# Kernel optimization log

Measured on AMD Instinct MI355X. Metric: run time of the kernel, lower is better.

Reference implementation:

```python
import jax, jax.numpy as jnp
import numpy as np

B, F, S, K = 4, 1024, 2048, 7


def _activate_norm(x):
    # relu -> mean-center over last dim -> L2-normalize scaled by sqrt(n)
    out = jax.nn.relu(x)
    out = out - jnp.mean(out, axis=-1, keepdims=True)
    n = out.shape[-1]
    denom = (jnp.sqrt(jnp.sum(out * out, axis=-1, keepdims=True)) + 1e-5) * (n ** -0.5)
    return out / denom


def _causal_conv(x, w, k):
    # x: [B, C_in, S], w: [C_out, C_in, k]; left-pad by k-1 for causality
    return jax.lax.conv_general_dilated(
        x, w, window_strides=(1,), padding=[(k - 1, 0)],
        dimension_numbers=('NCH', 'OIH', 'NCH'))


def _feed_forward(x, w0, w1, k):
    return _causal_conv(_activate_norm(_causal_conv(x, w0, k)), w1, k)


def setup_inputs() -> dict:
    key = jax.random.key(0)
    ks = jax.random.split(key, 8)
    scale = 0.02
    inp = jax.random.normal(ks[0], (B, F, S), dtype=jnp.float32)
    pos_embd = jax.random.normal(ks[1], (1, F, S), dtype=jnp.float32) * scale
    divisor = jnp.arange(1, F + 1, dtype=jnp.float32).reshape(1, F, 1)
    ws = [jax.random.normal(ks[2 + i], (F, F, K), dtype=jnp.float32) * scale
          for i in range(6)]
    return {
        'inp': inp, 'pos_embd': pos_embd, 'divisor': divisor,
        'depth_w0': ws[0], 'depth_w1': ws[1],
        'point_w0': ws[2], 'point_w1': ws[3],
        'shift_w0': ws[4], 'shift_w1': ws[5],
    }


def reference(inp, pos_embd, divisor, depth_w0, depth_w1, point_w0, point_w1, shift_w0, shift_w1):
    out = inp + pos_embd
    depth = _feed_forward(out, depth_w0, depth_w1, K)
    point = _feed_forward(out, point_w0, point_w1, K)
    shift = _feed_forward(out, shift_w0, shift_w1, K)
    # linear attention: cumsum over feature axis (dim 1), matching depth.cumsum(1)
    return _activate_norm(inp * (jnp.cumsum(depth, axis=1) / divisor + point) + shift)
```

## Files before the change

kernel.cpp:

```cpp
#include <hip/hip_runtime.h>
#include <hip/hip_bf16.h>
#include <stdint.h>

#define B_ 4
#define F_ 1024
#define S_ 2048
#define K_ 7
#define SP_ (S_ + K_ - 1)
#define FC_ 64
#define NC_ (F_ / FC_)
#define FF_ ((size_t)F_ * F_)
#define BFS_ ((size_t)B_ * F_ * S_)
#define BSPF_ ((size_t)B_ * SP_ * F_)
#define NT_ 112

using f32x4 = __attribute__((ext_vector_type(4))) float;
using s16x8 = __attribute__((ext_vector_type(8))) short;
using bf16 = __hip_bfloat16;

typedef const __attribute__((address_space(1))) void gvoid_t;
typedef __attribute__((address_space(3))) void lvoid_t;
__device__ __forceinline__ void async16(const void* g, void* l) {
    __builtin_amdgcn_global_load_lds((gvoid_t*)g, (lvoid_t*)l, 16, 0, 0);
}

__device__ __forceinline__ float bf2f(unsigned short u) {
    union { unsigned int i; float f; } c; c.i = ((unsigned int)u) << 16; return c.f;
}

#define FENCE() asm volatile("" ::: "memory")
#define BARRIER() do { FENCE(); __builtin_amdgcn_s_barrier(); FENCE(); } while (0)

__global__ void zero_pads(bf16* xT, bf16* hT, int nh) {
    int i = blockIdx.x * 256 + threadIdx.x;
    const int per = B_ * (K_ - 1) * F_;
    int total = (1 + nh) * per;
    if (i >= total) return;
    int r = i / per, o = i % per;
    int b = o / ((K_ - 1) * F_);
    int rr = o % ((K_ - 1) * F_);
    bf16 z = __float2bfloat16(0.0f);
    if (r == 0) xT[(size_t)b * SP_ * F_ + rr] = z;
    else        hT[(size_t)(r - 1) * BSPF_ + (size_t)b * SP_ * F_ + rr] = z;
}

__global__ void prep_x(const float* __restrict__ inp, const float* __restrict__ pos,
                       bf16* __restrict__ xT) {
    __shared__ bf16 tile[64][66];
    int b = blockIdx.z;
    int f0 = blockIdx.y * 64, s0 = blockIdx.x * 64;
    int tj = threadIdx.x & 63;
    int t4 = threadIdx.x >> 6;
#pragma unroll
    for (int r = 0; r < 16; ++r) {
        int i = r * 4 + t4;
        size_t off = (size_t)(f0 + i) * S_ + s0 + tj;
        float v = inp[(size_t)b * F_ * S_ + off] + pos[off];
        tile[i][tj] = __float2bfloat16(v);
    }
    __syncthreads();
#pragma unroll
    for (int r = 0; r < 16; ++r) {
        int j = r * 4 + t4;
        xT[(size_t)b * SP_ * F_ + (size_t)(6 + s0 + j) * F_ + f0 + tj] = tile[tj][j];
    }
}

__global__ void wconv(const float* __restrict__ w, bf16* __restrict__ wt) {
    int i = blockIdx.x * 256 + threadIdx.x;
    if (i >= F_ * F_) return;
    const float* src = w + (size_t)i * K_;
#pragma unroll
    for (int t = 0; t < K_; ++t)
        wt[(size_t)t * FF_ + i] = __float2bfloat16(src[t]);
}

#define MFMA_QUAD(MB, NB)                                                        \
    __builtin_amdgcn_s_setprio(1);                                               \
    _Pragma("unroll")                                                            \
    for (int kk = 0; kk < 2; ++kk) {                                             \
        _Pragma("unroll")                                                        \
        for (int m = 0; m < 4; ++m) {                                            \
            _Pragma("unroll")                                                    \
            for (int n = 0; n < 2; ++n) {                                        \
                acc[(MB) + m][(NB) + n] = __builtin_amdgcn_mfma_f32_16x16x32_bf16( \
                    af[m][kk], bfr[(NB) + n][kk], acc[(MB) + m][(NB) + n], 0, 0, 0); \
            }                                                                    \
        }                                                                        \
    }                                                                            \
    __builtin_amdgcn_s_setprio(0)

__global__ __launch_bounds__(512, 2)
void conv_gemm8(const bf16* __restrict__ Wbase, const bf16* __restrict__ Xbase,
                bf16* __restrict__ Obase, long wStride, long xStride, long oStride) {
    __shared__ __align__(16) char lds[147456];

    int wg = blockIdx.x;
    int swz = (wg & 7) * 48 + (wg >> 3);
    int nt = swz & 7;
    int mt = (swz >> 3) & 3;
    int z  = swz >> 5;
    int j = z >> 2, b = z & 3;

    const bf16* Wbr = Wbase + (size_t)j * wStride;
    const bf16* Xbr = Xbase + (size_t)j * xStride + (size_t)b * SP_ * F_;
    bf16* out = Obase + (size_t)j * oStride + (size_t)b * F_ * S_;
    const int m0 = mt * 256, n0 = nt * 256;

    const int tid = threadIdx.x;
    const int lane = tid & 63, wid = tid >> 6;
    const int wm = wid >> 2, wn = wid & 3;

    const int tid16 = tid * 16;
    const int p0 = tid16, p1 = 8192 + tid16;
    const int lp0 = p0 ^ (((p0 >> 9) & 1) << 5);
    const int lp1 = p1 ^ (((p1 >> 9) & 1) << 5);
    const int stgO0 = (((lp0 >> 11) << 4) + ((lp0 >> 6) & 15)) * F_
                    + (((lp0 >> 10) & 1) << 5) + ((lp0 & 63) >> 1);
    const int stgO1 = (((lp1 >> 11) << 4) + ((lp1 >> 6) & 15)) * F_
                    + (((lp1 >> 10) & 1) << 5) + ((lp1 & 63) >> 1);
    const int bsrc = (((tid16 >> 11) << 4) + ((lp0 >> 6) & 15)) * F_
                   + (((lp0 >> 10) & 1) << 5) + ((lp0 & 63) >> 1);

    const int rA = lane & 15, cA = (lane >> 4) * 8;
    const int swzRC = (rA << 6) + ((cA << 1) ^ (((rA >> 3) & 1) << 5));
    const int aOffBase = wm * 16384 + swzRC;
    int addrB[7];
#pragma unroll
    for (int t = 0; t < 7; ++t) {
        int R = wn * 64 + rA + t;
        addrB[t] = ((R >> 4) << 11) + ((R & 15) << 6)
                 + ((cA << 1) ^ (((R >> 3) & 1) << 5));
    }

    f32x4 acc[8][4] = {};
    s16x8 af[4][2], bfr[4][2];

    auto STGA = [&](int regionByte, const bf16* src) {
        async16(src + stgO0, lds + regionByte + tid16);
        async16(src + stgO1, lds + regionByte + 8192 + tid16);
    };
    auto STGB = [&](int kb1, int pc) {
        const bf16* src = Xbr + (size_t)n0 * F_ + kb1 * 64 + bsrc + pc * 64 * F_;
        async16(src, lds + 65536 + (kb1 & 1) * 40960 + pc * 8192 + tid16);
    };
    auto ASRC = [&](int kb, int t, int h) {
        return Wbr + (size_t)t * FF_ + (size_t)(m0 + h * 128) * F_ + kb * 64;
    };

    STGB(0, 0); STGB(0, 1); STGB(0, 2); STGB(0, 3); STGB(0, 4);
    STGA(0,     ASRC(0, 0, 0));
    STGA(16384, ASRC(0, 0, 1));
    STGA(32768, ASRC(0, 1, 0));
    asm volatile("s_waitcnt vmcnt(2)" ::: "memory");
    BARRIER();

    for (int kb = 0; kb < 16; ++kb) {
        const int bB = 65536 + (kb & 1) * 40960;
#pragma unroll
        for (int t = 0; t < 7; ++t) {
            const int kt = kb * 7 + t;
            const int pA = (kb + t) & 1;
            const char* la = lds + pA * 32768 + aOffBase;
            const char* lb = lds + bB + addrB[t];
            const int t1 = (t == 6) ? 0 : t + 1;
            const int kb1 = (t == 6) ? kb + 1 : kb;
            const int t2 = (t >= 5) ? t - 5 : t + 2;
            const int kb2 = (t >= 5) ? kb + 1 : kb;

#pragma unroll
            for (int m = 0; m < 4; ++m) {
                af[m][0] = *(const s16x8*)(la + m * 2048);
                af[m][1] = *(const s16x8*)(la + m * 2048 + 1024);
            }
#pragma unroll
            for (int n = 0; n < 2; ++n) {
                bfr[n][0] = *(const s16x8*)(lb + n * 2048);
                bfr[n][1] = *(const s16x8*)(lb + n * 2048 + 1024);
            }
            if (kt + 1 < NT_) STGA((pA ^ 1) * 32768 + 16384, ASRC(kb1, t1, 1));
            BARRIER();
            MFMA_QUAD(0, 0);
            BARRIER();

#pragma unroll
            for (int n = 0; n < 2; ++n) {
                bfr[2 + n][0] = *(const s16x8*)(lb + (2 + n) * 2048);
                bfr[2 + n][1] = *(const s16x8*)(lb + (2 + n) * 2048 + 1024);
            }
            if (t >= 1 && t <= 5) { if (kb < 15) STGB(kb + 1, t - 1); }
            BARRIER();
            MFMA_QUAD(0, 2);
            BARRIER();

#pragma unroll
            for (int m = 0; m < 4; ++m) {
                af[m][0] = *(const s16x8*)(la + (4 + m) * 2048);
                af[m][1] = *(const s16x8*)(la + (4 + m) * 2048 + 1024);
            }
            BARRIER();
            MFMA_QUAD(4, 0);
            BARRIER();

            if (kt + 2 < NT_) STGA(pA * 32768, ASRC(kb2, t2, 0));
            MFMA_QUAD(4, 2);
            if (kt < NT_ - 2) {
                if (t >= 1 && t <= 5 && kb < 15) {
                    asm volatile("s_waitcnt vmcnt(3)" ::: "memory");
                } else {
                    asm volatile("s_waitcnt vmcnt(2)" ::: "memory");
                }
            } else {
                asm volatile("s_waitcnt vmcnt(0)" ::: "memory");
            }
            BARRIER();
        }
    }

    const int cm = (lane >> 4) * 4, cn = lane & 15;
#pragma unroll
    for (int mf = 0; mf < 8; ++mf)
#pragma unroll
        for (int nf = 0; nf < 4; ++nf)
#pragma unroll
            for (int r = 0; r < 4; ++r) {
                int rr = m0 + wm * 128 + mf * 16 + cm + r;
                int cc = n0 + wn * 64 + nf * 16 + cn;
                out[(size_t)rr * S_ + cc] = __float2bfloat16(acc[mf][nf][r]);
            }
}

__global__ void conv_gemm_small(const bf16* __restrict__ W7, const bf16* __restrict__ xT,
                                bf16* __restrict__ out) {
    __shared__ bf16 tA[128][64];
    __shared__ bf16 tB[128][64];
    int wg = blockIdx.x;
    int cpx = gridDim.x >> 3;
    int swz = (wg & 7) * cpx + (wg >> 3);
    int sx = swz & 15;
    int t1 = swz >> 4;
    int sy = t1 & 7;
    int b = t1 >> 3;
    const bf16* Xbr = xT + (size_t)b * SP_ * F_;
    bf16* ob = out + (size_t)b * F_ * S_;
    int m0 = sy * 128, n0 = sx * 128;
    int tid = threadIdx.x;
    int lane = tid & 63, wid = tid >> 6;
    int wm = wid >> 1, wn = wid & 1;
    f32x4 acc[4][4] = {};
    int srow = tid >> 3, cpart = tid & 7;
    for (int t = 0; t < K_; ++t) {
        const bf16* Wt = W7 + (size_t)t * FF_ + (size_t)m0 * F_;
        const bf16* Xt = Xbr + (size_t)(n0 + t) * F_;
        for (int kb = 0; kb < F_ / 64; ++kb) {
            const bf16* wa = Wt + kb * 64 + cpart * 8;
            const bf16* xa = Xt + kb * 64 + cpart * 8;
#pragma unroll
            for (int q = 0; q < 4; ++q) async16(wa + (size_t)(q * 32 + srow) * F_, &tA[q * 32 + srow][cpart * 8]);
#pragma unroll
            for (int q = 0; q < 4; ++q) async16(xa + (size_t)(q * 32 + srow) * F_, &tB[q * 32 + srow][cpart * 8]);
            __syncthreads();
#pragma unroll
            for (int kk = 0; kk < 2; ++kk) {
                int krow = kk * 32 + (lane >> 4) * 8;
                s16x8 a2[4], b2[4];
#pragma unroll
                for (int m = 0; m < 4; ++m) a2[m] = *(const s16x8*)&tA[wm * 64 + m * 16 + (lane & 15)][krow];
#pragma unroll
                for (int n = 0; n < 4; ++n) b2[n] = *(const s16x8*)&tB[wn * 64 + n * 16 + (lane & 15)][krow];
#pragma unroll
                for (int m = 0; m < 4; ++m)
#pragma unroll
                    for (int n = 0; n < 4; ++n)
                        acc[m][n] = __builtin_amdgcn_mfma_f32_16x16x32_bf16(a2[m], b2[n], acc[m][n], 0, 0, 0);
            }
            __syncthreads();
        }
    }
    int cm = (lane >> 4) * 4, cn = lane & 15;
#pragma unroll
    for (int m = 0; m < 4; ++m)
#pragma unroll
        for (int n = 0; n < 4; ++n)
#pragma unroll
            for (int r = 0; r < 4; ++r)
                ob[(size_t)(m0 + wm * 64 + m * 16 + cm + r) * S_ + n0 + wn * 64 + n * 16 + cn] =
                    __float2bfloat16(acc[m][n][r]);
}

__global__ void rowstats_bf16(const bf16* __restrict__ x, float2* __restrict__ stats) {
    int row = blockIdx.x * 4 + (threadIdx.x >> 6);
    int lane = threadIdx.x & 63;
    const bf16* p = x + (size_t)row * S_;
    float s1 = 0.f, s2 = 0.f;
#pragma unroll
    for (int q = 0; q < S_ / 512; ++q) {
        s16x8 v = *(const s16x8*)(p + q * 512 + lane * 8);
#pragma unroll
        for (int e = 0; e < 8; ++e) {
            float f = fmaxf(bf2f((unsigned short)v[e]), 0.f);
            s1 += f; s2 += f * f;
        }
    }
#pragma unroll
    for (int d = 32; d; d >>= 1) { s1 += __shfl_xor(s1, d); s2 += __shfl_xor(s2, d); }
    if (lane == 0) {
        float m = s1 / (float)S_;
        float ss = fmaxf(s2 - (float)S_ * m * m, 0.f);
        float denom = (sqrtf(ss) + 1e-5f) * (1.0f / sqrtf((float)S_));
        stats[row] = make_float2(m, 1.0f / denom);
    }
}

__global__ void rowstats_f32(const float* __restrict__ x, float2* __restrict__ stats) {
    int row = blockIdx.x * 4 + (threadIdx.x >> 6);
    int lane = threadIdx.x & 63;
    const float* p = x + (size_t)row * S_;
    float s1 = 0.f, s2 = 0.f;
#pragma unroll
    for (int q = 0; q < S_; q += 256) {
        float4 v = *(const float4*)(p + q + lane * 4);
        float a = fmaxf(v.x, 0.f), bb = fmaxf(v.y, 0.f);
        float c = fmaxf(v.z, 0.f), d = fmaxf(v.w, 0.f);
        s1 += a + bb + c + d;
        s2 += a * a + bb * bb + c * c + d * d;
    }
#pragma unroll
    for (int d = 32; d; d >>= 1) { s1 += __shfl_xor(s1, d); s2 += __shfl_xor(s2, d); }
    if (lane == 0) {
        float m = s1 / (float)S_;
        float ss = fmaxf(s2 - (float)S_ * m * m, 0.f);
        float denom = (sqrtf(ss) + 1e-5f) * (1.0f / sqrtf((float)S_));
        stats[row] = make_float2(m, 1.0f / denom);
    }
}

__global__ void normT(const bf16* __restrict__ x, const float2* __restrict__ stats,
                      bf16* __restrict__ hT) {
    __shared__ bf16 tile[64][72];
    int z = blockIdx.z;
    int f0 = blockIdx.y * 64, s0 = blockIdx.x * 64;
    const bf16* xb = x + (size_t)z * F_ * S_;
    bf16* hb = hT + (size_t)z * SP_ * F_;
    const float2* st = stats + (size_t)z * F_;
    int i = threadIdx.x >> 3;
    int c8 = threadIdx.x & 7;
#pragma unroll
    for (int p = 0; p < 2; ++p) {
        int r = i + p * 32;
        float2 s = st[f0 + r];
        s16x8 v = *(const s16x8*)(xb + (size_t)(f0 + r) * S_ + s0 + c8 * 8);
#pragma unroll
        for (int e = 0; e < 8; ++e) {
            float f = fmaxf(bf2f((unsigned short)v[e]), 0.f);
            tile[r][c8 * 8 + e] = __float2bfloat16((f - s.x) * s.y);
        }
    }
    __syncthreads();
    int tj = threadIdx.x & 63;
    int t4 = threadIdx.x >> 6;
#pragma unroll
    for (int r = 0; r < 16; ++r) {
        int jrow = r * 4 + t4;
        hb[(size_t)(6 + s0 + jrow) * F_ + f0 + tj] = tile[tj][jrow];
    }
}

__global__ void combine_partial(const bf16* __restrict__ depth,
                                float* __restrict__ partials) {
    int idx = blockIdx.x * 256 + threadIdx.x;
    int s = idx & (S_ - 1);
    int t = idx / S_;
    int fc = t % NC_;
    int b = t / NC_;
    const bf16* p = depth + (size_t)b * F_ * S_ + (size_t)(fc * FC_) * S_ + s;
    float acc = 0.f;
#pragma unroll
    for (int f = 0; f < FC_; ++f) acc += __bfloat162float(p[(size_t)f * S_]);
    partials[idx] = acc;
}

__global__ void combine_apply(const float* __restrict__ inp, const float* __restrict__ divisor,
                              const bf16* __restrict__ depth, const bf16* __restrict__ point,
                              const bf16* __restrict__ shiftb,
                              const float* __restrict__ partials, float* __restrict__ y) {
    int idx = blockIdx.x * 256 + threadIdx.x;
    int s = idx & (S_ - 1);
    int t = idx / S_;
    int fc = t % NC_;
    int b = t / NC_;
    float acc = 0.f;
    const float* pp = partials + (size_t)b * NC_ * S_ + s;
    for (int c = 0; c < fc; ++c) acc += pp[(size_t)c * S_];
    size_t base = (size_t)b * F_ * S_ + (size_t)(fc * FC_) * S_ + s;
#pragma unroll 4
    for (int f = 0; f < FC_; ++f) {
        size_t o = base + (size_t)f * S_;
        acc += __bfloat162float(depth[o]);
        float yv = inp[o] * (acc / divisor[fc * FC_ + f] + __bfloat162float(point[o]))
                 + __bfloat162float(shiftb[o]);
        y[o] = yv;
    }
}

__global__ void finalnorm(const float* __restrict__ y, const float2* __restrict__ stats,
                          float* __restrict__ out) {
    size_t i = (size_t)blockIdx.x * 256 + threadIdx.x;
    if (i >= (size_t)B_ * F_ * S_) return;
    float2 st = stats[i / S_];
    float v = fmaxf(y[i], 0.f);
    out[i] = (v - st.x) * st.y;
}

extern "C" void kernel_launch(void* const* d_in, const int* in_sizes, int n_in,
                              void* d_out, int out_size, void* d_ws, size_t ws_size,
                              hipStream_t stream) {
    const float* inp = (const float*)d_in[0];
    const float* pos = (const float*)d_in[1];
    const float* divisor = (const float*)d_in[2];
    const float* w[6] = { (const float*)d_in[3], (const float*)d_in[4],
                          (const float*)d_in[5], (const float*)d_in[6],
                          (const float*)d_in[7], (const float*)d_in[8] };
    float* out = (float*)d_out;

    size_t off = 0;
    auto alloc = [&](size_t bytes) {
        off = (off + 255) & ~(size_t)255;
        void* r = (char*)d_ws + off;
        off += bytes;
        return r;
    };

    const size_t needB = ((BSPF_ * 2 + 255) & ~255UL)
                       + ((3 * BSPF_ * 2 + 255) & ~255UL)
                       + ((3 * 7 * FF_ * 2 + 255) & ~255UL)
                       + ((3 * BFS_ * 2 + 255) & ~255UL)
                       + ((3 * BFS_ * 2 + 255) & ~255UL)
                       + ((3 * B_ * F_ * 8 + 255) & ~255UL)
                       + ((B_ * NC_ * S_ * 4 + 255) & ~255UL)
                       + 4096;

    if (ws_size >= needB) {
        bf16* xT   = (bf16*)alloc(BSPF_ * 2);
        bf16* hT3  = (bf16*)alloc(3 * BSPF_ * 2);
        bf16* Wb3  = (bf16*)alloc(3 * 7 * FF_ * 2);
        bf16* O3   = (bf16*)alloc(3 * BFS_ * 2);
        bf16* br3  = (bf16*)alloc(3 * BFS_ * 2);
        float2* stats3 = (float2*)alloc(3 * B_ * F_ * 8);
        float* partials = (float*)alloc(B_ * NC_ * S_ * 4);
        float* ybuf = (float*)O3;

        zero_pads<<<(4 * B_ * (K_ - 1) * F_ + 255) / 256, 256, 0, stream>>>(xT, hT3, 3);
        prep_x<<<dim3(S_ / 64, F_ / 64, B_), 256, 0, stream>>>(inp, pos, xT);

        for (int j = 0; j < 3; ++j)
            wconv<<<F_ * F_ / 256, 256, 0, stream>>>(w[2 * j], Wb3 + j * 7 * FF_);
        conv_gemm8<<<384, 512, 0, stream>>>(Wb3, xT, O3, 7 * FF_, 0, BFS_);
        rowstats_bf16<<<3 * B_ * F_ / 4, 256, 0, stream>>>(O3, stats3);
        normT<<<dim3(S_ / 64, F_ / 64, 12), 256, 0, stream>>>(O3, stats3, hT3);

        for (int j = 0; j < 3; ++j)
            wconv<<<F_ * F_ / 256, 256, 0, stream>>>(w[2 * j + 1], Wb3 + j * 7 * FF_);
        conv_gemm8<<<384, 512, 0, stream>>>(Wb3, hT3, br3, 7 * FF_, BSPF_, BFS_);

        combine_partial<<<B_ * NC_ * S_ / 256, 256, 0, stream>>>(br3, partials);
        combine_apply<<<B_ * NC_ * S_ / 256, 256, 0, stream>>>(
            inp, divisor, br3, br3 + BFS_, br3 + 2 * BFS_, partials, ybuf);
        rowstats_f32<<<B_ * F_ / 4, 256, 0, stream>>>(ybuf, stats3);
        finalnorm<<<(B_ * F_ * S_) / 256, 256, 0, stream>>>(ybuf, stats3, out);
    } else {
        bf16* xT   = (bf16*)alloc(BSPF_ * 2);
        bf16* hT1  = (bf16*)alloc(BSPF_ * 2);
        bf16* Wb1  = (bf16*)alloc(7 * FF_ * 2);
        bf16* O1   = (bf16*)alloc(BFS_ * 2);
        bf16* br3  = (bf16*)alloc(3 * BFS_ * 2);
        float2* stats3 = (float2*)alloc(B_ * F_ * 8);
        float* partials = (float*)alloc(B_ * NC_ * S_ * 4);
        float* ybuf = (float*)xT;

        zero_pads<<<(2 * B_ * (K_ - 1) * F_ + 255) / 256, 256, 0, stream>>>(xT, hT1, 1);
        prep_x<<<dim3(S_ / 64, F_ / 64, B_), 256, 0, stream>>>(inp, pos, xT);

        for (int j = 0; j < 3; ++j) {
            wconv<<<F_ * F_ / 256, 256, 0, stream>>>(w[2 * j], Wb1);
            conv_gemm_small<<<16 * 8 * 4, 256, 0, stream>>>(Wb1, xT, O1);
            rowstats_bf16<<<B_ * F_ / 4, 256, 0, stream>>>(O1, stats3);
            normT<<<dim3(S_ / 64, F_ / 64, 4), 256, 0, stream>>>(O1, stats3, hT1);
            wconv<<<F_ * F_ / 256, 256, 0, stream>>>(w[2 * j + 1], Wb1);
            conv_gemm_small<<<16 * 8 * 4, 256, 0, stream>>>(Wb1, hT1, br3 + j * BFS_);
        }
        combine_partial<<<B_ * NC_ * S_ / 256, 256, 0, stream>>>(br3, partials);
        combine_apply<<<B_ * NC_ * S_ / 256, 256, 0, stream>>>(
            inp, divisor, br3, br3 + BFS_, br3 + 2 * BFS_, partials, ybuf);
        rowstats_f32<<<B_ * F_ / 4, 256, 0, stream>>>(ybuf, stats3);
        finalnorm<<<(B_ * F_ * S_) / 256, 256, 0, stream>>>(ybuf, stats3, out);
    }
}
```

Measured before the change: 795.5 us.

## Split conv GEMM reduction into two K halves with a bf16 add pass

The big conv GEMM kernel is templated to split its 16 K-blocks into two halves. This doubles the grid from 384 to 768 workgroups so the GPU's compute units are better filled. Each half writes a bf16 partial to a separate buffer, and a new elementwise kernel adds them. The trade-off is an extra buffer, an extra pass over the outputs, and double rounding of the partial sums to bf16. The split only runs when the workspace is large enough.

```diff
diff --git a/kernel.cpp b/kernel.cpp
--- a/kernel.cpp
+++ b/kernel.cpp
@@ -12,7 +12,6 @@
 #define FF_ ((size_t)F_ * F_)
 #define BFS_ ((size_t)B_ * F_ * S_)
 #define BSPF_ ((size_t)B_ * SP_ * F_)
-#define NT_ 112
 
 using f32x4 = __attribute__((ext_vector_type(4))) float;
 using s16x8 = __attribute__((ext_vector_type(8))) short;
@@ -90,21 +89,29 @@
     }                                                                            \
     __builtin_amdgcn_s_setprio(0)
 
+template <bool SPLIT>
 __global__ __launch_bounds__(512, 2)
 void conv_gemm8(const bf16* __restrict__ Wbase, const bf16* __restrict__ Xbase,
-                bf16* __restrict__ Obase, long wStride, long xStride, long oStride) {
+                bf16* __restrict__ O0, bf16* __restrict__ O1,
+                long wStride, long xStride, long oStride) {
     __shared__ __align__(16) char lds[147456];
 
     int wg = blockIdx.x;
-    int swz = (wg & 7) * 48 + (wg >> 3);
-    int nt = swz & 7;
-    int mt = (swz >> 3) & 3;
-    int z  = swz >> 5;
+    int nchunk = gridDim.x >> 3;
+    int swz = (wg & 7) * nchunk + (wg >> 3);
+    int kp, r;
+    if (SPLIT) { kp = swz & 1; r = swz >> 1; } else { kp = 0; r = swz; }
+    int nt = r & 7;
+    int mt = (r >> 3) & 3;
+    int z  = r >> 5;
     int j = z >> 2, b = z & 3;
+    const int kb0 = kp * 8;
+    const int kbN = SPLIT ? 8 : 16;
+    const int NTp = kbN * 7;
 
     const bf16* Wbr = Wbase + (size_t)j * wStride;
     const bf16* Xbr = Xbase + (size_t)j * xStride + (size_t)b * SP_ * F_;
-    bf16* out = Obase + (size_t)j * oStride + (size_t)b * F_ * S_;
+    bf16* out = (kp ? O1 : O0) + (size_t)j * oStride + (size_t)b * F_ * S_;
     const int m0 = mt * 256, n0 = nt * 256;
 
     const int tid = threadIdx.x;
@@ -148,18 +155,18 @@
         return Wbr + (size_t)t * FF_ + (size_t)(m0 + h * 128) * F_ + kb * 64;
     };
 
-    STGB(0, 0); STGB(0, 1); STGB(0, 2); STGB(0, 3); STGB(0, 4);
-    STGA(0,     ASRC(0, 0, 0));
-    STGA(16384, ASRC(0, 0, 1));
-    STGA(32768, ASRC(0, 1, 0));
+    STGB(kb0, 0); STGB(kb0, 1); STGB(kb0, 2); STGB(kb0, 3); STGB(kb0, 4);
+    STGA(0,     ASRC(kb0, 0, 0));
+    STGA(16384, ASRC(kb0, 0, 1));
+    STGA(32768, ASRC(kb0, 1, 0));
     asm volatile("s_waitcnt vmcnt(2)" ::: "memory");
     BARRIER();
 
-    for (int kb = 0; kb < 16; ++kb) {
+    for (int kb = kb0; kb < kb0 + kbN; ++kb) {
         const int bB = 65536 + (kb & 1) * 40960;
 #pragma unroll
         for (int t = 0; t < 7; ++t) {
-            const int kt = kb * 7 + t;
+            const int ktl = (kb - kb0) * 7 + t;
             const int pA = (kb + t) & 1;
             const char* la = lds + pA * 32768 + aOffBase;
             const char* lb = lds + bB + addrB[t];
@@ -167,6 +174,7 @@
             const int kb1 = (t == 6) ? kb + 1 : kb;
             const int t2 = (t >= 5) ? t - 5 : t + 2;
             const int kb2 = (t >= 5) ? kb + 1 : kb;
+            const bool bstage = (t >= 1 && t <= 5) && (kb - kb0) < kbN - 1;
 
 #pragma unroll
             for (int m = 0; m < 4; ++m) {
@@ -178,7 +186,7 @@
                 bfr[n][0] = *(const s16x8*)(lb + n * 2048);
                 bfr[n][1] = *(const s16x8*)(lb + n * 2048 + 1024);
             }
-            if (kt + 1 < NT_) STGA((pA ^ 1) * 32768 + 16384, ASRC(kb1, t1, 1));
+            if (ktl + 1 < NTp) STGA((pA ^ 1) * 32768 + 16384, ASRC(kb1, t1, 1));
             BARRIER();
             MFMA_QUAD(0, 0);
             BARRIER();
@@ -188,7 +196,7 @@
                 bfr[2 + n][0] = *(const s16x8*)(lb + (2 + n) * 2048);
                 bfr[2 + n][1] = *(const s16x8*)(lb + (2 + n) * 2048 + 1024);
             }
-            if (t >= 1 && t <= 5) { if (kb < 15) STGB(kb + 1, t - 1); }
+            if (bstage) STGB(kb + 1, t - 1);
             BARRIER();
             MFMA_QUAD(0, 2);
             BARRIER();
@@ -202,14 +210,11 @@
             MFMA_QUAD(4, 0);
             BARRIER();
 
-            if (kt + 2 < NT_) STGA(pA * 32768, ASRC(kb2, t2, 0));
+            if (ktl + 2 < NTp) STGA(pA * 32768, ASRC(kb2, t2, 0));
             MFMA_QUAD(4, 2);
-            if (kt < NT_ - 2) {
-                if (t >= 1 && t <= 5 && kb < 15) {
-                    asm volatile("s_waitcnt vmcnt(3)" ::: "memory");
-                } else {
-                    asm volatile("s_waitcnt vmcnt(2)" ::: "memory");
-                }
+            if (ktl < NTp - 2) {
+                if (bstage) { asm volatile("s_waitcnt vmcnt(3)" ::: "memory"); }
+                else        { asm volatile("s_waitcnt vmcnt(2)" ::: "memory"); }
             } else {
                 asm volatile("s_waitcnt vmcnt(0)" ::: "memory");
             }
@@ -223,11 +228,25 @@
 #pragma unroll
         for (int nf = 0; nf < 4; ++nf)
 #pragma unroll
-            for (int r = 0; r < 4; ++r) {
-                int rr = m0 + wm * 128 + mf * 16 + cm + r;
+            for (int r2 = 0; r2 < 4; ++r2) {
+                int rr = m0 + wm * 128 + mf * 16 + cm + r2;
                 int cc = n0 + wn * 64 + nf * 16 + cn;
-                out[(size_t)rr * S_ + cc] = __float2bfloat16(acc[mf][nf][r]);
-            }
+                out[(size_t)rr * S_ + cc] = __float2bfloat16(acc[mf][nf][r2]);
+            }
+}
+
+__global__ void addb(const bf16* __restrict__ a, bf16* __restrict__ d, long n8) {
+    long i = (long)blockIdx.x * 256 + threadIdx.x;
+    if (i >= n8) return;
+    s16x8 va = ((const s16x8*)a)[i];
+    s16x8 vd = ((const s16x8*)d)[i];
+    s16x8 o;
+#pragma unroll
+    for (int e = 0; e < 8; ++e) {
+        float f = bf2f((unsigned short)va[e]) + bf2f((unsigned short)vd[e]);
+        o[e] = (short)__bfloat16_as_ushort(__float2bfloat16(f));
+    }
+    ((s16x8*)d)[i] = o;
 }
 
 __global__ void conv_gemm_small(const bf16* __restrict__ W7, const bf16* __restrict__ xT,
@@ -439,8 +458,10 @@
                        + ((3 * B_ * F_ * 8 + 255) & ~255UL)
                        + ((B_ * NC_ * S_ * 4 + 255) & ~255UL)
                        + 4096;
+    const size_t needC = needB + ((3 * BFS_ * 2 + 255) & ~255UL);
 
     if (ws_size >= needB) {
+        const bool splitK = (ws_size >= needC);
         bf16* xT   = (bf16*)alloc(BSPF_ * 2);
         bf16* hT3  = (bf16*)alloc(3 * BSPF_ * 2);
         bf16* Wb3  = (bf16*)alloc(3 * 7 * FF_ * 2);
@@ -448,20 +469,32 @@
         bf16* br3  = (bf16*)alloc(3 * BFS_ * 2);
         float2* stats3 = (float2*)alloc(3 * B_ * F_ * 8);
         float* partials = (float*)alloc(B_ * NC_ * S_ * 4);
+        bf16* P0 = splitK ? (bf16*)alloc(3 * BFS_ * 2) : nullptr;
         float* ybuf = (float*)O3;
+        const long n8 = (long)(3 * BFS_ / 8);
 
         zero_pads<<<(4 * B_ * (K_ - 1) * F_ + 255) / 256, 256, 0, stream>>>(xT, hT3, 3);
         prep_x<<<dim3(S_ / 64, F_ / 64, B_), 256, 0, stream>>>(inp, pos, xT);
 
         for (int j = 0; j < 3; ++j)
             wconv<<<F_ * F_ / 256, 256, 0, stream>>>(w[2 * j], Wb3 + j * 7 * FF_);
-        conv_gemm8<<<384, 512, 0, stream>>>(Wb3, xT, O3, 7 * FF_, 0, BFS_);
+        if (splitK) {
+            conv_gemm8<true><<<768, 512, 0, stream>>>(Wb3, xT, P0, O3, 7 * FF_, 0, BFS_);
+            addb<<<(int)(n8 / 256), 256, 0, stream>>>(P0, O3, n8);
+        } else {
+            conv_gemm8<false><<<384, 512, 0, stream>>>(Wb3, xT, O3, O3, 7 * FF_, 0, BFS_);
+        }
         rowstats_bf16<<<3 * B_ * F_ / 4, 256, 0, stream>>>(O3, stats3);
         normT<<<dim3(S_ / 64, F_ / 64, 12), 256, 0, stream>>>(O3, stats3, hT3);
 
         for (int j = 0; j < 3; ++j)
             wconv<<<F_ * F_ / 256, 256, 0, stream>>>(w[2 * j + 1], Wb3 + j * 7 * FF_);
-        conv_gemm8<<<384, 512, 0, stream>>>(Wb3, hT3, br3, 7 * FF_, BSPF_, BFS_);
+        if (splitK) {
+            conv_gemm8<true><<<768, 512, 0, stream>>>(Wb3, hT3, P0, br3, 7 * FF_, BSPF_, BFS_);
+            addb<<<(int)(n8 / 256), 256, 0, stream>>>(P0, br3, n8);
+        } else {
+            conv_gemm8<false><<<384, 512, 0, stream>>>(Wb3, hT3, br3, br3, 7 * FF_, BSPF_, BFS_);
+        }
 
         combine_partial<<<B_ * NC_ * S_ / 256, 256, 0, stream>>>(br3, partials);
         combine_apply<<<B_ * NC_ * S_ / 256, 256, 0, stream>>>(
```

After: 737.3 us. -7.3%, faster.
